# Optimization experiments

Hardware: AMD Instinct MI355X
Metric: run time of the kernel (lower is better)

The kernel has to match this reference:

```python
import jax, jax.numpy as jnp
import numpy as np
import math


def setup_inputs() -> dict:
    key = jax.random.key(0)
    kq, kk, kv = jax.random.split(key, 3)
    B, N, H = 4, 4096, 128
    return {
        "q": jax.random.normal(kq, (B, N, H), dtype=jnp.float32),
        "k": jax.random.normal(kk, (B, N, H), dtype=jnp.float32),
        "v": jax.random.normal(kv, (B, N, H), dtype=jnp.float32),
        "block_size": 128,
    }


def reference(q, k, v, block_size):
    # The torch module is an exact online-softmax (flash-attention) tiling of
    # full, unmasked softmax attention: out = softmax(q k^T / sqrt(H)) @ v.
    # The block-wise m/l running updates compute the identical result, so the
    # clean dense form below is the faithful math.
    H = q.shape[-1]
    scale = 1.0 / math.sqrt(H)
    s = jnp.einsum("bnh,bmh->bnm", q, k) * scale  # [B, N, N]
    p = jax.nn.softmax(s, axis=-1)                 # numerically stable softmax
    return jnp.einsum("bnm,bmh->bnh", p, v)
```

## Files before the change

### kernel.cpp

```cpp
#include <hip/hip_runtime.h>

typedef __attribute__((ext_vector_type(4)))  float f32x4;
typedef __attribute__((ext_vector_type(16))) float f32x16;
typedef __attribute__((ext_vector_type(8)))  short short8;

#define DEVI static __device__ __forceinline__

constexpr int B_ = 4;
constexpr int N_ = 4096;
constexpr int H_ = 128;
constexpr size_t ELEMS = (size_t)B_ * N_ * H_;
constexpr size_t TSB = ELEMS * 2;

constexpr int QT = 128;
constexpr int KVB = 32;
constexpr int NTH = 256;

DEVI unsigned short f2bf(float x) {
  union { float f; unsigned u; } a; a.f = x;
  unsigned u = a.u;
  return (unsigned short)((u + 0x7FFFu + ((u >> 16) & 1u)) >> 16);
}

DEVI unsigned cvt_pk_bf16(float lo, float hi) {
  unsigned w;
  asm("v_cvt_pk_bf16_f32 %0, %1, %2" : "=v"(w) : "v"(lo), "v"(hi));
  return w;
}

DEVI void gl_lds16(const void* g, void* l) {
  __builtin_amdgcn_global_load_lds(
      (const __attribute__((address_space(1))) void*)g,
      (__attribute__((address_space(3))) void*)l, 16, 0, 0);
}

__global__ void conv_qk(const float* __restrict__ q, const float* __restrict__ k,
                        unsigned short* __restrict__ qb, unsigned short* __restrict__ kb) {
  const float qscale = 0.08838834764831845f * 1.4426950408889634f;
  size_t i = (size_t)blockIdx.x * blockDim.x + threadIdx.x;
  {
    const float4* s = (const float4*)q + 2 * i;
    float4 a = s[0], b = s[1];
    short8 t;
    t[0] = (short)f2bf(a.x * qscale); t[1] = (short)f2bf(a.y * qscale);
    t[2] = (short)f2bf(a.z * qscale); t[3] = (short)f2bf(a.w * qscale);
    t[4] = (short)f2bf(b.x * qscale); t[5] = (short)f2bf(b.y * qscale);
    t[6] = (short)f2bf(b.z * qscale); t[7] = (short)f2bf(b.w * qscale);
    *(short8*)(qb + i * 8) = t;
  }
  {
    const float4* s = (const float4*)k + 2 * i;
    float4 a = s[0], b = s[1];
    short8 t;
    t[0] = (short)f2bf(a.x); t[1] = (short)f2bf(a.y);
    t[2] = (short)f2bf(a.z); t[3] = (short)f2bf(a.w);
    t[4] = (short)f2bf(b.x); t[5] = (short)f2bf(b.y);
    t[6] = (short)f2bf(b.z); t[7] = (short)f2bf(b.w);
    *(short8*)(kb + i * 8) = t;
  }
}

__global__ void conv_vt(const float* __restrict__ v, unsigned short* __restrict__ vt) {
  __shared__ unsigned short T[64][72];
  const int n0 = blockIdx.x * 64, h0 = blockIdx.y * 64, b = blockIdx.z;
  const int t = threadIdx.x;
  const int c4 = t & 15, r = t >> 4;
#pragma unroll
  for (int i = 0; i < 4; ++i) {
    int n = n0 + r + 16 * i;
    float4 val = *(const float4*)(v + ((size_t)b * N_ + n) * H_ + h0 + 4 * c4);
    T[4 * c4 + 0][r + 16 * i] = f2bf(val.x);
    T[4 * c4 + 1][r + 16 * i] = f2bf(val.y);
    T[4 * c4 + 2][r + 16 * i] = f2bf(val.z);
    T[4 * c4 + 3][r + 16 * i] = f2bf(val.w);
  }
  __syncthreads();
  const int c8 = t & 7, hr = t >> 3;
#pragma unroll
  for (int i = 0; i < 2; ++i) {
    int hl = hr + 32 * i;
    short8 val = *(const short8*)(&T[hl][8 * c8]);
    *(short8*)(vt + ((size_t)b * H_ + h0 + hl) * N_ + n0 + 8 * c8) = val;
  }
}

template <int KS>
__global__ __launch_bounds__(NTH, 2)
void fattn_v8(const unsigned short* __restrict__ qws,
              const unsigned short* __restrict__ kws,
              const unsigned short* __restrict__ vtws,
              float* __restrict__ opart, float* __restrict__ mlpart) {
  constexpr int KVRANGE = N_ / KS;
  constexpr int NST = KVRANGE / KVB;
  constexpr int PPX = (B_ * KS) / 8;

  __shared__ __align__(16) char smem[36864];
  char* Kb0 = smem;
  char* Vb0 = smem + 16384;

  const int tid = threadIdx.x, wave = tid >> 6, lane = tid & 63;
  const int l31 = lane & 31, half = lane >> 5;

  const int bid = blockIdx.x;
  const int pair = (bid & 7) * PPX + ((bid >> 3) & (PPX - 1));
  const int x = bid >> (3 + (PPX == 4 ? 2 : (PPX == 2 ? 1 : 0)));
  const int b = pair / KS, z = pair % KS;

  const int qg0 = x * QT + wave * 32;
  const size_t kvz = (size_t)z * KVRANGE;

  const unsigned short* qp0 = qws + ((size_t)b * N_ + qg0 + l31) * H_ + 8 * half;
  short8 qf[8];
#pragma unroll
  for (int c = 0; c < 8; ++c) qf[c] = *(const short8*)(qp0 + 16 * c);

  f32x16 O0 = {}, O1 = {}, O2 = {}, O3 = {};
  float m = 0.f, l = 0.f;

  const char* kbase = (const char*)(kws + ((size_t)b * N_ + kvz) * H_);
  const char* vbase = (const char*)(vtws + (size_t)b * H_ * N_) + kvz * 2;

  const int vh = tid >> 1;
  const int vc = (tid & 1) * 2;

  {
#pragma unroll
    for (int i = 0; i < 2; ++i) {
      int off = (tid + 256 * i) * 16;
      int row = off >> 8, col = off & 255;
      gl_lds16(kbase + row * 256 + (col ^ ((row & 15) << 4)), Kb0 + off);
    }
    uint4 vr0 = *(const uint4*)(vbase + (size_t)vh * (N_ * 2) + vc * 16);
    uint4 vr1 = *(const uint4*)(vbase + (size_t)vh * (N_ * 2) + vc * 16 + 16);
    *(uint4*)(Vb0 + vh * 80 + vc * 16) = vr0;
    *(uint4*)(Vb0 + vh * 80 + vc * 16 + 16) = vr1;
  }
  __syncthreads();
  int cur = 0;

  const int kcol = 16 * half;
  const int kswz = (lane & 15) << 4;

  for (int st = 0; st < NST; ++st) {
    uint4 vr0, vr1;
    if (st + 1 < NST) {
      const char* kt = kbase + (size_t)(st + 1) * KVB * H_ * 2;
      char* kd = Kb0 + (cur ^ 1) * 8192;
#pragma unroll
      for (int i = 0; i < 2; ++i) {
        int off = (tid + 256 * i) * 16;
        int row = off >> 8, col = off & 255;
        gl_lds16(kt + row * 256 + (col ^ ((row & 15) << 4)), kd + off);
      }
      const char* vt0 = vbase + (size_t)(st + 1) * KVB * 2;
      vr0 = *(const uint4*)(vt0 + (size_t)vh * (N_ * 2) + vc * 16);
      vr1 = *(const uint4*)(vt0 + (size_t)vh * (N_ * 2) + vc * 16 + 16);
    }

    const char* Kl = Kb0 + cur * 8192;
    const char* Vl = Vb0 + cur * 10240;

    f32x16 S = {};
    __builtin_amdgcn_s_setprio(1);
#pragma unroll
    for (int c = 0; c < 8; ++c) {
      short8 af = *(const short8*)(Kl + l31 * 256 + ((32 * c + kcol) ^ kswz));
      S = __builtin_amdgcn_mfma_f32_32x32x16_bf16(af, qf[c], S, 0, 0, 0);
    }
    __builtin_amdgcn_s_setprio(0);

    float p[16];
#pragma unroll
    for (int i = 0; i < 16; ++i) p[i] = __builtin_amdgcn_exp2f(S[i] - m);
    float mx01 = fmaxf(p[0], p[1]),  mx23 = fmaxf(p[2], p[3]);
    float mx45 = fmaxf(p[4], p[5]),  mx67 = fmaxf(p[6], p[7]);
    float mx89 = fmaxf(p[8], p[9]),  mxab = fmaxf(p[10], p[11]);
    float mxcd = fmaxf(p[12], p[13]), mxef = fmaxf(p[14], p[15]);
    float mx = fmaxf(fmaxf(fmaxf(mx01, mx23), fmaxf(mx45, mx67)),
                     fmaxf(fmaxf(mx89, mxab), fmaxf(mxcd, mxef)));
    mx = fmaxf(mx, __shfl_xor(mx, 32));
    float rs = (((p[0] + p[1]) + (p[2] + p[3])) + ((p[4] + p[5]) + (p[6] + p[7]))) +
               (((p[8] + p[9]) + (p[10] + p[11])) + ((p[12] + p[13]) + (p[14] + p[15])));
    rs += __shfl_xor(rs, 32);
    if (__builtin_expect(!__all(mx <= 256.f), 0)) {
      float sc = fmaxf(mx, 1.f);
      float ai = 1.f / sc;
      m += __builtin_amdgcn_logf(sc);
      l = (l + rs) * ai;
#pragma unroll
      for (int i = 0; i < 16; ++i) p[i] *= ai;
#pragma unroll
      for (int i = 0; i < 16; ++i) { O0[i] *= ai; O1[i] *= ai; O2[i] *= ai; O3[i] *= ai; }
    } else {
      l += rs;
    }

    unsigned u0 = cvt_pk_bf16(p[0], p[1]),  u1 = cvt_pk_bf16(p[2], p[3]);
    unsigned u2 = cvt_pk_bf16(p[4], p[5]),  u3 = cvt_pk_bf16(p[6], p[7]);
    unsigned u4 = cvt_pk_bf16(p[8], p[9]),  u5 = cvt_pk_bf16(p[10], p[11]);
    unsigned u6 = cvt_pk_bf16(p[12], p[13]), u7 = cvt_pk_bf16(p[14], p[15]);
    unsigned ra = __shfl_xor((int)(half ? u0 : u2), 32);
    unsigned rb = __shfl_xor((int)(half ? u1 : u3), 32);
    unsigned rc = __shfl_xor((int)(half ? u4 : u6), 32);
    unsigned rd = __shfl_xor((int)(half ? u5 : u7), 32);
    union { unsigned u[4]; short8 s; } f0, f1;
    f0.u[0] = half ? ra : u0;  f0.u[1] = half ? rb : u1;
    f0.u[2] = half ? u2 : ra;  f0.u[3] = half ? u3 : rb;
    f1.u[0] = half ? rc : u4;  f1.u[1] = half ? rd : u5;
    f1.u[2] = half ? u6 : rc;  f1.u[3] = half ? u7 : rd;

    __builtin_amdgcn_s_setprio(1);
    {
      const char* vrow = Vl + l31 * 80 + 16 * half;
      short8 a00 = *(const short8*)(vrow + 0 * 2560);
      short8 a10 = *(const short8*)(vrow + 1 * 2560);
      short8 a20 = *(const short8*)(vrow + 2 * 2560);
      short8 a30 = *(const short8*)(vrow + 3 * 2560);
      O0 = __builtin_amdgcn_mfma_f32_32x32x16_bf16(a00, f0.s, O0, 0, 0, 0);
      O1 = __builtin_amdgcn_mfma_f32_32x32x16_bf16(a10, f0.s, O1, 0, 0, 0);
      O2 = __builtin_amdgcn_mfma_f32_32x32x16_bf16(a20, f0.s, O2, 0, 0, 0);
      O3 = __builtin_amdgcn_mfma_f32_32x32x16_bf16(a30, f0.s, O3, 0, 0, 0);
      short8 a01 = *(const short8*)(vrow + 32 + 0 * 2560);
      short8 a11 = *(const short8*)(vrow + 32 + 1 * 2560);
      short8 a21 = *(const short8*)(vrow + 32 + 2 * 2560);
      short8 a31 = *(const short8*)(vrow + 32 + 3 * 2560);
      O0 = __builtin_amdgcn_mfma_f32_32x32x16_bf16(a01, f1.s, O0, 0, 0, 0);
      O1 = __builtin_amdgcn_mfma_f32_32x32x16_bf16(a11, f1.s, O1, 0, 0, 0);
      O2 = __builtin_amdgcn_mfma_f32_32x32x16_bf16(a21, f1.s, O2, 0, 0, 0);
      O3 = __builtin_amdgcn_mfma_f32_32x32x16_bf16(a31, f1.s, O3, 0, 0, 0);
    }
    __builtin_amdgcn_s_setprio(0);

    if (st + 1 < NST) {
      char* vd = Vb0 + (cur ^ 1) * 10240;
      *(uint4*)(vd + vh * 80 + vc * 16) = vr0;
      *(uint4*)(vd + vh * 80 + vc * 16 + 16) = vr1;
    }
    __syncthreads();
    cur ^= 1;
  }

  const size_t zb = (size_t)z * B_ + b;
  if (half == 0) {
    float2 ml = {m, l};
    *(float2*)(mlpart + 2 * (zb * N_ + qg0 + l31)) = ml;
  }
  float* od = opart + (zb * N_ + qg0 + l31) * H_ + 4 * half;
#pragma unroll
  for (int g = 0; g < 4; ++g) {
    f32x4 v0 = {O0[4 * g], O0[4 * g + 1], O0[4 * g + 2], O0[4 * g + 3]};
    f32x4 v1 = {O1[4 * g], O1[4 * g + 1], O1[4 * g + 2], O1[4 * g + 3]};
    f32x4 v2 = {O2[4 * g], O2[4 * g + 1], O2[4 * g + 2], O2[4 * g + 3]};
    f32x4 v3 = {O3[4 * g], O3[4 * g + 1], O3[4 * g + 2], O3[4 * g + 3]};
    *(f32x4*)(od + 8 * g) = v0;
    *(f32x4*)(od + 32 + 8 * g) = v1;
    *(f32x4*)(od + 64 + 8 * g) = v2;
    *(f32x4*)(od + 96 + 8 * g) = v3;
  }
}

template <int KS>
__global__ void combine_k(const float* __restrict__ opart, const float* __restrict__ mlpart,
                          float* __restrict__ out) {
  const int t = threadIdx.x;
  size_t row = (size_t)blockIdx.x * 8 + (t >> 5);
  int hc = (t & 31) * 4;
  float mz[KS], lz[KS];
  float mi = -__builtin_inff();
#pragma unroll
  for (int z = 0; z < KS; ++z) {
    size_t r = (size_t)z * B_ * N_ + row;
    mz[z] = mlpart[2 * r];
    lz[z] = mlpart[2 * r + 1];
    mi = fmaxf(mi, mz[z]);
  }
  float lsum = 0.f;
  float az[KS];
#pragma unroll
  for (int z = 0; z < KS; ++z) {
    az[z] = __builtin_amdgcn_exp2f(mz[z] - mi);
    lsum += az[z] * lz[z];
  }
  float rinv = 1.f / lsum;
  f32x4 acc = {};
#pragma unroll
  for (int z = 0; z < KS; ++z) {
    f32x4 oz = *(const f32x4*)(opart + (size_t)z * B_ * N_ * H_ + row * H_ + hc);
    acc = acc + oz * (az[z] * rinv);
  }
  *(f32x4*)(out + row * H_ + hc) = acc;
}

constexpr int FB_QTILE = 64;
constexpr int FB_KVSTEP = 128;
constexpr int FB_KVHALF = 64;
constexpr int FB_NTH = 512;
constexpr int FB_NSTEPS = N_ / FB_KVSTEP;

__global__ __launch_bounds__(FB_NTH, 2)
void fattn_fast(const unsigned short* __restrict__ qws,
                const unsigned short* __restrict__ kws,
                const unsigned short* __restrict__ vtws,
                float* __restrict__ out) {
  __shared__ unsigned short Kbuf[2][FB_KVSTEP * H_];
  __shared__ unsigned short Vbuf[2][H_ * FB_KVSTEP];
  __shared__ unsigned short Plds[8][16 * FB_KVHALF];
  __shared__ float MLlds[4][16][2];

  const int tid = threadIdx.x;
  const int wave = tid >> 6;
  const int lane = tid & 63;
  const int l15 = lane & 15;
  const int l4 = lane >> 4;
  const int sub = wave & 3;
  const int grp = wave >> 2;

  const int b = blockIdx.y;
  const int qbase = blockIdx.x * FB_QTILE;

  const unsigned short* qp = qws + ((size_t)b * N_ + qbase + sub * 16 + l15) * H_;
  short8 qfrag[4];
#pragma unroll
  for (int kc = 0; kc < 4; ++kc)
    qfrag[kc] = *(const short8*)(qp + 8 * l4 + 32 * kc);

  f32x4 Oacc[8];
#pragma unroll
  for (int i = 0; i < 8; ++i) Oacc[i] = (f32x4){0.f, 0.f, 0.f, 0.f};
  float mrun[4], lrun[4];
#pragma unroll
  for (int r = 0; r < 4; ++r) { mrun[r] = -__builtin_inff(); lrun[r] = 0.f; }

  const char* kbase = (const char*)(kws + (size_t)b * N_ * H_);
  const char* vbase = (const char*)(vtws + (size_t)b * H_ * N_);
  const int kvbase = grp * FB_KVHALF;
  char* pbase = (char*)Plds[wave];

  auto stage = [&](int buf, int step) {
    const char* ktile = kbase + (size_t)step * FB_KVSTEP * H_ * 2;
#pragma unroll
    for (int i = 0; i < 4; ++i) {
      int chunk = wave * 4 + i;
      int off = chunk * 1024 + lane * 16;
      int row = off >> 8, col = off & 255;
      gl_lds16(ktile + row * 256 + (col ^ ((row & 7) << 4)),
               (char*)Kbuf[buf] + chunk * 1024);
    }
#pragma unroll
    for (int i = 0; i < 4; ++i) {
      int chunk = wave * 4 + i;
      int h = chunk * 4 + (lane >> 4);
      int colb = (lane & 15) * 16;
      gl_lds16(vbase + (size_t)h * (N_ * 2) + (size_t)step * 256 + (colb ^ ((h & 7) << 4)),
               (char*)Vbuf[buf] + chunk * 1024);
    }
  };

  int cur = 0;
  stage(0, 0);
  __syncthreads();

  for (int step = 0; step < FB_NSTEPS; ++step) {
    if (step + 1 < FB_NSTEPS) stage(cur ^ 1, step + 1);

    const char* Kl = (const char*)Kbuf[cur];
    const char* Vl = (const char*)Vbuf[cur];

    f32x4 S[4];
#pragma unroll
    for (int ct = 0; ct < 4; ++ct) S[ct] = (f32x4){0.f, 0.f, 0.f, 0.f};
#pragma unroll
    for (int ct = 0; ct < 4; ++ct) {
      int kvrow = kvbase + ct * 16 + l15;
#pragma unroll
      for (int kc = 0; kc < 4; ++kc) {
        short8 bfrag = *(const short8*)(Kl +
            ((kvrow * 256 + (8 * l4 + 32 * kc) * 2) ^ ((kvrow & 7) << 4)));
        S[ct] = __builtin_amdgcn_mfma_f32_16x16x32_bf16(qfrag[kc], bfrag, S[ct], 0, 0, 0);
      }
    }

    float mnew[4];
#pragma unroll
    for (int r = 0; r < 4; ++r) {
      float mx = fmaxf(fmaxf(S[0][r], S[1][r]), fmaxf(S[2][r], S[3][r]));
      mx = fmaxf(mx, __shfl_xor(mx, 1));
      mx = fmaxf(mx, __shfl_xor(mx, 2));
      mx = fmaxf(mx, __shfl_xor(mx, 4));
      mx = fmaxf(mx, __shfl_xor(mx, 8));
      mnew[r] = mx;
    }
    float alpha[4];
#pragma unroll
    for (int r = 0; r < 4; ++r) {
      float mi = fmaxf(mrun[r], mnew[r]);
      alpha[r] = __builtin_amdgcn_exp2f(mrun[r] - mi);
      mrun[r] = mi;
    }
    float rsum[4] = {0.f, 0.f, 0.f, 0.f};
    unsigned short pb[4][4];
#pragma unroll
    for (int ct = 0; ct < 4; ++ct)
#pragma unroll
      for (int r = 0; r < 4; ++r) {
        float pv = __builtin_amdgcn_exp2f(S[ct][r] - mrun[r]);
        rsum[r] += pv;
        pb[ct][r] = f2bf(pv);
      }
#pragma unroll
    for (int r = 0; r < 4; ++r) {
      float s = rsum[r];
      s += __shfl_xor(s, 1); s += __shfl_xor(s, 2);
      s += __shfl_xor(s, 4); s += __shfl_xor(s, 8);
      lrun[r] = lrun[r] * alpha[r] + s;
    }
#pragma unroll
    for (int ct2 = 0; ct2 < 8; ++ct2)
#pragma unroll
      for (int r = 0; r < 4; ++r) Oacc[ct2][r] *= alpha[r];

#pragma unroll
    for (int ct = 0; ct < 4; ++ct)
#pragma unroll
      for (int r = 0; r < 4; ++r) {
        int qrow = 4 * l4 + r;
        int kv = l15 + 16 * ct;
        *(unsigned short*)(pbase + ((qrow * 128 + kv * 2) ^ ((qrow & 7) << 4))) = pb[ct][r];
      }

#pragma unroll
    for (int kc2 = 0; kc2 < 2; ++kc2) {
      short8 afrag = *(const short8*)(pbase +
          ((l15 * 128 + (8 * l4 + 32 * kc2) * 2) ^ ((l15 & 7) << 4)));
#pragma unroll
      for (int ct2 = 0; ct2 < 8; ++ct2) {
        int h = l15 + 16 * ct2;
        short8 bfrag = *(const short8*)(Vl +
            ((h * 256 + (kvbase + 8 * l4 + 32 * kc2) * 2) ^ ((h & 7) << 4)));
        Oacc[ct2] = __builtin_amdgcn_mfma_f32_16x16x32_bf16(afrag, bfrag, Oacc[ct2], 0, 0, 0);
      }
    }

    __syncthreads();
    cur ^= 1;
  }

  __syncthreads();
  float* mergeO = (float*)Kbuf;
  if (grp == 1) {
#pragma unroll
    for (int ct2 = 0; ct2 < 8; ++ct2)
#pragma unroll
      for (int r = 0; r < 4; ++r) {
        int qrow = 4 * l4 + r, h = l15 + 16 * ct2;
        mergeO[(sub * 16 + qrow) * H_ + h] = Oacc[ct2][r];
      }
    if (l15 == 0) {
#pragma unroll
      for (int r = 0; r < 4; ++r) {
        int qrow = 4 * l4 + r;
        MLlds[sub][qrow][0] = mrun[r];
        MLlds[sub][qrow][1] = lrun[r];
      }
    }
  }
  __syncthreads();
  if (grp == 0) {
    float aA[4], aB[4], rl[4];
#pragma unroll
    for (int r = 0; r < 4; ++r) {
      int qrow = 4 * l4 + r;
      float mB = MLlds[sub][qrow][0], lB = MLlds[sub][qrow][1];
      float mi = fmaxf(mrun[r], mB);
      aA[r] = __builtin_amdgcn_exp2f(mrun[r] - mi);
      aB[r] = __builtin_amdgcn_exp2f(mB - mi);
      rl[r] = 1.f / (lrun[r] * aA[r] + lB * aB[r]);
    }
    float* outp = out + ((size_t)b * N_ + qbase + sub * 16) * H_;
#pragma unroll
    for (int ct2 = 0; ct2 < 8; ++ct2)
#pragma unroll
      for (int r = 0; r < 4; ++r) {
        int qrow = 4 * l4 + r, h = l15 + 16 * ct2;
        float ob = mergeO[(sub * 16 + qrow) * H_ + h];
        outp[(size_t)qrow * H_ + h] = (Oacc[ct2][r] * aA[r] + ob * aB[r]) * rl[r];
      }
  }
}

extern "C" void kernel_launch(void* const* d_in, const int* in_sizes, int n_in,
                              void* d_out, int out_size, void* d_ws, size_t ws_size,
                              hipStream_t stream) {
  const float* q = (const float*)d_in[0];
  const float* k = (const float*)d_in[1];
  const float* v = (const float*)d_in[2];
  float* out = (float*)d_out;

  auto need = [](int ks) {
    return 3 * TSB + (size_t)ks * ELEMS * 4 + (size_t)ks * B_ * N_ * 2 * 4;
  };

  unsigned short* qb = (unsigned short*)d_ws;
  unsigned short* kb = qb + ELEMS;
  unsigned short* vt = kb + ELEMS;

  if (ws_size >= need(4)) {
    float* opart = (float*)((char*)d_ws + 3 * TSB);
    float* mlpart = opart + (size_t)4 * ELEMS;
    conv_qk<<<dim3((unsigned)(ELEMS / 8 / 256)), dim3(256), 0, stream>>>(q, k, qb, kb);
    conv_vt<<<dim3(N_ / 64, H_ / 64, B_), dim3(256), 0, stream>>>(v, vt);
    fattn_v8<4><<<dim3(32 * B_ * 4), dim3(NTH), 0, stream>>>(qb, kb, vt, opart, mlpart);
    combine_k<4><<<dim3(B_ * N_ / 8), dim3(256), 0, stream>>>(opart, mlpart, out);
  } else if (ws_size >= need(2)) {
    float* opart = (float*)((char*)d_ws + 3 * TSB);
    float* mlpart = opart + (size_t)2 * ELEMS;
    conv_qk<<<dim3((unsigned)(ELEMS / 8 / 256)), dim3(256), 0, stream>>>(q, k, qb, kb);
    conv_vt<<<dim3(N_ / 64, H_ / 64, B_), dim3(256), 0, stream>>>(v, vt);
    fattn_v8<2><<<dim3(32 * B_ * 2), dim3(NTH), 0, stream>>>(qb, kb, vt, opart, mlpart);
    combine_k<2><<<dim3(B_ * N_ / 8), dim3(256), 0, stream>>>(opart, mlpart, out);
  } else if (ws_size >= 3 * TSB) {
    conv_qk<<<dim3((unsigned)(ELEMS / 8 / 256)), dim3(256), 0, stream>>>(q, k, qb, kb);
    conv_vt<<<dim3(N_ / 64, H_ / 64, B_), dim3(256), 0, stream>>>(v, vt);
    fattn_fast<<<dim3(N_ / FB_QTILE, B_), dim3(FB_NTH), 0, stream>>>(qb, kb, vt, out);
  }
}
```

Baseline: 75.17 us.

## Double KV block to 64 and fuse conversion kernels into one launch

```diff
diff --git a/kernel.cpp b/kernel.cpp
--- a/kernel.cpp
+++ b/kernel.cpp
@@ -13,7 +13,7 @@
 constexpr size_t TSB = ELEMS * 2;
 
 constexpr int QT = 128;
-constexpr int KVB = 32;
+constexpr int KVB = 64;
 constexpr int NTH = 256;
 
 DEVI unsigned short f2bf(float x) {
@@ -34,59 +34,63 @@
       (__attribute__((address_space(3))) void*)l, 16, 0, 0);
 }
 
-__global__ void conv_qk(const float* __restrict__ q, const float* __restrict__ k,
-                        unsigned short* __restrict__ qb, unsigned short* __restrict__ kb) {
-  const float qscale = 0.08838834764831845f * 1.4426950408889634f;
-  size_t i = (size_t)blockIdx.x * blockDim.x + threadIdx.x;
-  {
-    const float4* s = (const float4*)q + 2 * i;
-    float4 a = s[0], b = s[1];
-    short8 t;
-    t[0] = (short)f2bf(a.x * qscale); t[1] = (short)f2bf(a.y * qscale);
-    t[2] = (short)f2bf(a.z * qscale); t[3] = (short)f2bf(a.w * qscale);
-    t[4] = (short)f2bf(b.x * qscale); t[5] = (short)f2bf(b.y * qscale);
-    t[6] = (short)f2bf(b.z * qscale); t[7] = (short)f2bf(b.w * qscale);
-    *(short8*)(qb + i * 8) = t;
-  }
-  {
-    const float4* s = (const float4*)k + 2 * i;
-    float4 a = s[0], b = s[1];
-    short8 t;
-    t[0] = (short)f2bf(a.x); t[1] = (short)f2bf(a.y);
-    t[2] = (short)f2bf(a.z); t[3] = (short)f2bf(a.w);
-    t[4] = (short)f2bf(b.x); t[5] = (short)f2bf(b.y);
-    t[6] = (short)f2bf(b.z); t[7] = (short)f2bf(b.w);
-    *(short8*)(kb + i * 8) = t;
-  }
-}
-
-__global__ void conv_vt(const float* __restrict__ v, unsigned short* __restrict__ vt) {
+__global__ void conv_all(const float* __restrict__ q, const float* __restrict__ k,
+                         const float* __restrict__ v,
+                         unsigned short* __restrict__ qb, unsigned short* __restrict__ kb,
+                         unsigned short* __restrict__ vt) {
   __shared__ unsigned short T[64][72];
-  const int n0 = blockIdx.x * 64, h0 = blockIdx.y * 64, b = blockIdx.z;
+  const int bid = blockIdx.x;
   const int t = threadIdx.x;
-  const int c4 = t & 15, r = t >> 4;
-#pragma unroll
-  for (int i = 0; i < 4; ++i) {
-    int n = n0 + r + 16 * i;
-    float4 val = *(const float4*)(v + ((size_t)b * N_ + n) * H_ + h0 + 4 * c4);
-    T[4 * c4 + 0][r + 16 * i] = f2bf(val.x);
-    T[4 * c4 + 1][r + 16 * i] = f2bf(val.y);
-    T[4 * c4 + 2][r + 16 * i] = f2bf(val.z);
-    T[4 * c4 + 3][r + 16 * i] = f2bf(val.w);
-  }
-  __syncthreads();
-  const int c8 = t & 7, hr = t >> 3;
-#pragma unroll
-  for (int i = 0; i < 2; ++i) {
-    int hl = hr + 32 * i;
-    short8 val = *(const short8*)(&T[hl][8 * c8]);
-    *(short8*)(vt + ((size_t)b * H_ + h0 + hl) * N_ + n0 + 8 * c8) = val;
+  if (bid < 1024) {
+    const float qscale = 0.08838834764831845f * 1.4426950408889634f;
+    size_t i = (size_t)bid * 256 + t;
+    {
+      const float4* s = (const float4*)q + 2 * i;
+      float4 a = s[0], b = s[1];
+      short8 o;
+      o[0] = (short)f2bf(a.x * qscale); o[1] = (short)f2bf(a.y * qscale);
+      o[2] = (short)f2bf(a.z * qscale); o[3] = (short)f2bf(a.w * qscale);
+      o[4] = (short)f2bf(b.x * qscale); o[5] = (short)f2bf(b.y * qscale);
+      o[6] = (short)f2bf(b.z * qscale); o[7] = (short)f2bf(b.w * qscale);
+      *(short8*)(qb + i * 8) = o;
+    }
+    {
+      const float4* s = (const float4*)k + 2 * i;
+      float4 a = s[0], b = s[1];
+      short8 o;
+      o[0] = (short)f2bf(a.x); o[1] = (short)f2bf(a.y);
+      o[2] = (short)f2bf(a.z); o[3] = (short)f2bf(a.w);
+      o[4] = (short)f2bf(b.x); o[5] = (short)f2bf(b.y);
+      o[6] = (short)f2bf(b.z); o[7] = (short)f2bf(b.w);
+      *(short8*)(kb + i * 8) = o;
+    }
+  } else {
+    const int vb = bid - 1024;
+    const int n0 = (vb & 63) * 64, h0 = ((vb >> 6) & 1) * 64, b = vb >> 7;
+    const int c4 = t & 15, r = t >> 4;
+#pragma unroll
+    for (int i = 0; i < 4; ++i) {
+      int n = n0 + r + 16 * i;
+      float4 val = *(const float4*)(v + ((size_t)b * N_ + n) * H_ + h0 + 4 * c4);
+      T[4 * c4 + 0][r + 16 * i] = f2bf(val.x);
+      T[4 * c4 + 1][r + 16 * i] = f2bf(val.y);
+      T[4 * c4 + 2][r + 16 * i] = f2bf(val.z);
+      T[4 * c4 + 3][r + 16 * i] = f2bf(val.w);
+    }
+    __syncthreads();
+    const int c8 = t & 7, hr = t >> 3;
+#pragma unroll
+    for (int i = 0; i < 2; ++i) {
+      int hl = hr + 32 * i;
+      short8 val = *(const short8*)(&T[hl][8 * c8]);
+      *(short8*)(vt + ((size_t)b * H_ + h0 + hl) * N_ + n0 + 8 * c8) = val;
+    }
   }
 }
 
 template <int KS>
 __global__ __launch_bounds__(NTH, 2)
-void fattn_v8(const unsigned short* __restrict__ qws,
+void fattn_v9(const unsigned short* __restrict__ qws,
               const unsigned short* __restrict__ kws,
               const unsigned short* __restrict__ vtws,
               float* __restrict__ opart, float* __restrict__ mlpart) {
@@ -94,9 +98,9 @@
   constexpr int NST = KVRANGE / KVB;
   constexpr int PPX = (B_ * KS) / 8;
 
-  __shared__ __align__(16) char smem[36864];
+  __shared__ __align__(16) char smem[69632];
   char* Kb0 = smem;
-  char* Vb0 = smem + 16384;
+  char* Vb0 = smem + 32768;
 
   const int tid = threadIdx.x, wave = tid >> 6, lane = tid & 63;
   const int l31 = lane & 31, half = lane >> 5;
@@ -120,67 +124,71 @@
   const char* kbase = (const char*)(kws + ((size_t)b * N_ + kvz) * H_);
   const char* vbase = (const char*)(vtws + (size_t)b * H_ * N_) + kvz * 2;
 
-  const int vh = tid >> 1;
-  const int vc = (tid & 1) * 2;
+  const int vrow = tid >> 1;
+  const int vhb = (tid & 1) * 64;
 
   {
 #pragma unroll
-    for (int i = 0; i < 2; ++i) {
-      int off = (tid + 256 * i) * 16;
+    for (int i = 0; i < 4; ++i) {
+      int off = tid * 16 + 4096 * i;
       int row = off >> 8, col = off & 255;
       gl_lds16(kbase + row * 256 + (col ^ ((row & 15) << 4)), Kb0 + off);
     }
-    uint4 vr0 = *(const uint4*)(vbase + (size_t)vh * (N_ * 2) + vc * 16);
-    uint4 vr1 = *(const uint4*)(vbase + (size_t)vh * (N_ * 2) + vc * 16 + 16);
-    *(uint4*)(Vb0 + vh * 80 + vc * 16) = vr0;
-    *(uint4*)(Vb0 + vh * 80 + vc * 16 + 16) = vr1;
+    const char* vsrc = vbase + (size_t)vrow * (N_ * 2) + vhb;
+    char* vdst = Vb0 + vrow * 144 + vhb;
+#pragma unroll
+    for (int i = 0; i < 4; ++i)
+      *(uint4*)(vdst + 16 * i) = *(const uint4*)(vsrc + 16 * i);
   }
   __syncthreads();
   int cur = 0;
 
-  const int kcol = 16 * half;
-  const int kswz = (lane & 15) << 4;
+  const int kswz = (l31 & 15) << 4;
+  const int kcolb = 16 * half;
 
   for (int st = 0; st < NST; ++st) {
-    uint4 vr0, vr1;
+    uint4 vr[4];
     if (st + 1 < NST) {
       const char* kt = kbase + (size_t)(st + 1) * KVB * H_ * 2;
-      char* kd = Kb0 + (cur ^ 1) * 8192;
-#pragma unroll
-      for (int i = 0; i < 2; ++i) {
-        int off = (tid + 256 * i) * 16;
+      char* kd = Kb0 + (cur ^ 1) * 16384;
+#pragma unroll
+      for (int i = 0; i < 4; ++i) {
+        int off = tid * 16 + 4096 * i;
         int row = off >> 8, col = off & 255;
         gl_lds16(kt + row * 256 + (col ^ ((row & 15) << 4)), kd + off);
       }
-      const char* vt0 = vbase + (size_t)(st + 1) * KVB * 2;
-      vr0 = *(const uint4*)(vt0 + (size_t)vh * (N_ * 2) + vc * 16);
-      vr1 = *(const uint4*)(vt0 + (size_t)vh * (N_ * 2) + vc * 16 + 16);
-    }
-
-    const char* Kl = Kb0 + cur * 8192;
-    const char* Vl = Vb0 + cur * 10240;
-
-    f32x16 S = {};
+      const char* vsrc = vbase + (size_t)(st + 1) * KVB * 2 + (size_t)vrow * (N_ * 2) + vhb;
+#pragma unroll
+      for (int i = 0; i < 4; ++i) vr[i] = *(const uint4*)(vsrc + 16 * i);
+    }
+
+    const char* Kl = Kb0 + cur * 16384;
+    const char* Vl = Vb0 + cur * 18432;
+
+    f32x16 S0 = {}, S1 = {};
     __builtin_amdgcn_s_setprio(1);
 #pragma unroll
     for (int c = 0; c < 8; ++c) {
-      short8 af = *(const short8*)(Kl + l31 * 256 + ((32 * c + kcol) ^ kswz));
-      S = __builtin_amdgcn_mfma_f32_32x32x16_bf16(af, qf[c], S, 0, 0, 0);
+      short8 a0 = *(const short8*)(Kl + l31 * 256 + ((32 * c + kcolb) ^ kswz));
+      short8 a1 = *(const short8*)(Kl + (32 + l31) * 256 + ((32 * c + kcolb) ^ kswz));
+      S0 = __builtin_amdgcn_mfma_f32_32x32x16_bf16(a0, qf[c], S0, 0, 0, 0);
+      S1 = __builtin_amdgcn_mfma_f32_32x32x16_bf16(a1, qf[c], S1, 0, 0, 0);
     }
     __builtin_amdgcn_s_setprio(0);
 
-    float p[16];
-#pragma unroll
-    for (int i = 0; i < 16; ++i) p[i] = __builtin_amdgcn_exp2f(S[i] - m);
-    float mx01 = fmaxf(p[0], p[1]),  mx23 = fmaxf(p[2], p[3]);
-    float mx45 = fmaxf(p[4], p[5]),  mx67 = fmaxf(p[6], p[7]);
-    float mx89 = fmaxf(p[8], p[9]),  mxab = fmaxf(p[10], p[11]);
-    float mxcd = fmaxf(p[12], p[13]), mxef = fmaxf(p[14], p[15]);
-    float mx = fmaxf(fmaxf(fmaxf(mx01, mx23), fmaxf(mx45, mx67)),
-                     fmaxf(fmaxf(mx89, mxab), fmaxf(mxcd, mxef)));
+    float p[32];
+#pragma unroll
+    for (int i = 0; i < 16; ++i) p[i] = __builtin_amdgcn_exp2f(S0[i] - m);
+#pragma unroll
+    for (int i = 0; i < 16; ++i) p[16 + i] = __builtin_amdgcn_exp2f(S1[i] - m);
+    float mx = fmaxf(p[0], p[1]);
+    float rs = p[0] + p[1];
+#pragma unroll
+    for (int i = 2; i < 32; i += 2) {
+      mx = fmaxf(mx, fmaxf(p[i], p[i + 1]));
+      rs += p[i] + p[i + 1];
+    }
     mx = fmaxf(mx, __shfl_xor(mx, 32));
-    float rs = (((p[0] + p[1]) + (p[2] + p[3])) + ((p[4] + p[5]) + (p[6] + p[7]))) +
-               (((p[8] + p[9]) + (p[10] + p[11])) + ((p[12] + p[13]) + (p[14] + p[15])));
     rs += __shfl_xor(rs, 32);
     if (__builtin_expect(!__all(mx <= 256.f), 0)) {
       float sc = fmaxf(mx, 1.f);
@@ -188,53 +196,51 @@
       m += __builtin_amdgcn_logf(sc);
       l = (l + rs) * ai;
 #pragma unroll
-      for (int i = 0; i < 16; ++i) p[i] *= ai;
+      for (int i = 0; i < 32; ++i) p[i] *= ai;
 #pragma unroll
       for (int i = 0; i < 16; ++i) { O0[i] *= ai; O1[i] *= ai; O2[i] *= ai; O3[i] *= ai; }
     } else {
       l += rs;
     }
 
-    unsigned u0 = cvt_pk_bf16(p[0], p[1]),  u1 = cvt_pk_bf16(p[2], p[3]);
-    unsigned u2 = cvt_pk_bf16(p[4], p[5]),  u3 = cvt_pk_bf16(p[6], p[7]);
-    unsigned u4 = cvt_pk_bf16(p[8], p[9]),  u5 = cvt_pk_bf16(p[10], p[11]);
-    unsigned u6 = cvt_pk_bf16(p[12], p[13]), u7 = cvt_pk_bf16(p[14], p[15]);
-    unsigned ra = __shfl_xor((int)(half ? u0 : u2), 32);
-    unsigned rb = __shfl_xor((int)(half ? u1 : u3), 32);
-    unsigned rc = __shfl_xor((int)(half ? u4 : u6), 32);
-    unsigned rd = __shfl_xor((int)(half ? u5 : u7), 32);
-    union { unsigned u[4]; short8 s; } f0, f1;
-    f0.u[0] = half ? ra : u0;  f0.u[1] = half ? rb : u1;
-    f0.u[2] = half ? u2 : ra;  f0.u[3] = half ? u3 : rb;
-    f1.u[0] = half ? rc : u4;  f1.u[1] = half ? rd : u5;
-    f1.u[2] = half ? u6 : rc;  f1.u[3] = half ? u7 : rd;
+    short8 pf[4];
+#pragma unroll
+    for (int g = 0; g < 2; ++g) {
+      const float* pp = p + 16 * g;
+      unsigned u0 = cvt_pk_bf16(pp[0], pp[1]),   u1 = cvt_pk_bf16(pp[2], pp[3]);
+      unsigned u2 = cvt_pk_bf16(pp[4], pp[5]),   u3 = cvt_pk_bf16(pp[6], pp[7]);
+      unsigned u4 = cvt_pk_bf16(pp[8], pp[9]),   u5 = cvt_pk_bf16(pp[10], pp[11]);
+      unsigned u6 = cvt_pk_bf16(pp[12], pp[13]), u7 = cvt_pk_bf16(pp[14], pp[15]);
+      unsigned ra = __shfl_xor((int)(half ? u0 : u2), 32);
+      unsigned rb = __shfl_xor((int)(half ? u1 : u3), 32);
+      unsigned rc = __shfl_xor((int)(half ? u4 : u6), 32);
+      unsigned rd = __shfl_xor((int)(half ? u5 : u7), 32);
+      union { unsigned u[4]; short8 s; } f0, f1;
+      f0.u[0] = half ? ra : u0;  f0.u[1] = half ? rb : u1;
+      f0.u[2] = half ? u2 : ra;  f0.u[3] = half ? u3 : rb;
+      f1.u[0] = half ? rc : u4;  f1.u[1] = half ? rd : u5;
+      f1.u[2] = half ? u6 : rc;  f1.u[3] = half ? u7 : rd;
+      pf[2 * g] = f0.s;
+      pf[2 * g + 1] = f1.s;
+    }
 
     __builtin_amdgcn_s_setprio(1);
-    {
-      const char* vrow = Vl + l31 * 80 + 16 * half;
-      short8 a00 = *(const short8*)(vrow + 0 * 2560);
-      short8 a10 = *(const short8*)(vrow + 1 * 2560);
-      short8 a20 = *(const short8*)(vrow + 2 * 2560);
-      short8 a30 = *(const short8*)(vrow + 3 * 2560);
-      O0 = __builtin_amdgcn_mfma_f32_32x32x16_bf16(a00, f0.s, O0, 0, 0, 0);
-      O1 = __builtin_amdgcn_mfma_f32_32x32x16_bf16(a10, f0.s, O1, 0, 0, 0);
-      O2 = __builtin_amdgcn_mfma_f32_32x32x16_bf16(a20, f0.s, O2, 0, 0, 0);
-      O3 = __builtin_amdgcn_mfma_f32_32x32x16_bf16(a30, f0.s, O3, 0, 0, 0);
-      short8 a01 = *(const short8*)(vrow + 32 + 0 * 2560);
-      short8 a11 = *(const short8*)(vrow + 32 + 1 * 2560);
-      short8 a21 = *(const short8*)(vrow + 32 + 2 * 2560);
-      short8 a31 = *(const short8*)(vrow + 32 + 3 * 2560);
-      O0 = __builtin_amdgcn_mfma_f32_32x32x16_bf16(a01, f1.s, O0, 0, 0, 0);
-      O1 = __builtin_amdgcn_mfma_f32_32x32x16_bf16(a11, f1.s, O1, 0, 0, 0);
-      O2 = __builtin_amdgcn_mfma_f32_32x32x16_bf16(a21, f1.s, O2, 0, 0, 0);
-      O3 = __builtin_amdgcn_mfma_f32_32x32x16_bf16(a31, f1.s, O3, 0, 0, 0);
+#pragma unroll
+    for (int t2 = 0; t2 < 4; ++t2) {
+      const char* vp = Vl + (32 * t2 + l31) * 144 + 16 * half;
+      f32x16 acc = (t2 == 0) ? O0 : (t2 == 1) ? O1 : (t2 == 2) ? O2 : O3;
+      acc = __builtin_amdgcn_mfma_f32_32x32x16_bf16(*(const short8*)(vp), pf[0], acc, 0, 0, 0);
+      acc = __builtin_amdgcn_mfma_f32_32x32x16_bf16(*(const short8*)(vp + 32), pf[1], acc, 0, 0, 0);
+      acc = __builtin_amdgcn_mfma_f32_32x32x16_bf16(*(const short8*)(vp + 64), pf[2], acc, 0, 0, 0);
+      acc = __builtin_amdgcn_mfma_f32_32x32x16_bf16(*(const short8*)(vp + 96), pf[3], acc, 0, 0, 0);
+      if (t2 == 0) O0 = acc; else if (t2 == 1) O1 = acc; else if (t2 == 2) O2 = acc; else O3 = acc;
     }
     __builtin_amdgcn_s_setprio(0);
 
     if (st + 1 < NST) {
-      char* vd = Vb0 + (cur ^ 1) * 10240;
-      *(uint4*)(vd + vh * 80 + vc * 16) = vr0;
-      *(uint4*)(vd + vh * 80 + vc * 16 + 16) = vr1;
+      char* vdst = Vb0 + (cur ^ 1) * 18432 + vrow * 144 + vhb;
+#pragma unroll
+      for (int i = 0; i < 4; ++i) *(uint4*)(vdst + 16 * i) = vr[i];
     }
     __syncthreads();
     cur ^= 1;
@@ -507,20 +513,17 @@
   if (ws_size >= need(4)) {
     float* opart = (float*)((char*)d_ws + 3 * TSB);
     float* mlpart = opart + (size_t)4 * ELEMS;
-    conv_qk<<<dim3((unsigned)(ELEMS / 8 / 256)), dim3(256), 0, stream>>>(q, k, qb, kb);
-    conv_vt<<<dim3(N_ / 64, H_ / 64, B_), dim3(256), 0, stream>>>(v, vt);
-    fattn_v8<4><<<dim3(32 * B_ * 4), dim3(NTH), 0, stream>>>(qb, kb, vt, opart, mlpart);
+    conv_all<<<dim3(1536), dim3(256), 0, stream>>>(q, k, v, qb, kb, vt);
+    fattn_v9<4><<<dim3(32 * B_ * 4), dim3(NTH), 0, stream>>>(qb, kb, vt, opart, mlpart);
     combine_k<4><<<dim3(B_ * N_ / 8), dim3(256), 0, stream>>>(opart, mlpart, out);
   } else if (ws_size >= need(2)) {
     float* opart = (float*)((char*)d_ws + 3 * TSB);
     float* mlpart = opart + (size_t)2 * ELEMS;
-    conv_qk<<<dim3((unsigned)(ELEMS / 8 / 256)), dim3(256), 0, stream>>>(q, k, qb, kb);
-    conv_vt<<<dim3(N_ / 64, H_ / 64, B_), dim3(256), 0, stream>>>(v, vt);
-    fattn_v8<2><<<dim3(32 * B_ * 2), dim3(NTH), 0, stream>>>(qb, kb, vt, opart, mlpart);
+    conv_all<<<dim3(1536), dim3(256), 0, stream>>>(q, k, v, qb, kb, vt);
+    fattn_v9<2><<<dim3(32 * B_ * 2), dim3(NTH), 0, stream>>>(qb, kb, vt, opart, mlpart);
     combine_k<2><<<dim3(B_ * N_ / 8), dim3(256), 0, stream>>>(opart, mlpart, out);
   } else if (ws_size >= 3 * TSB) {
-    conv_qk<<<dim3((unsigned)(ELEMS / 8 / 256)), dim3(256), 0, stream>>>(q, k, qb, kb);
-    conv_vt<<<dim3(N_ / 64, H_ / 64, B_), dim3(256), 0, stream>>>(v, vt);
+    conv_all<<<dim3(1536), dim3(256), 0, stream>>>(q, k, v, qb, kb, vt);
     fattn_fast<<<dim3(N_ / FB_QTILE, B_), dim3(FB_NTH), 0, stream>>>(qb, kb, vt, out);
   }
 }
```

Result: slower. 77.27 us (+2.8%).
